# Kernel optimization log

Hardware: AMD Instinct MI355X
Metric: run time of the kernel (lower is better)

The kernel has to match this reference:

```python
import jax, jax.numpy as jnp
import numpy as np

N, E = 50000, 800000
H, C_IN, C_HID, C_OUT = 4, 256, 64, 64
NEG_SLOPE = 0.2


def leaky_relu(x, s=NEG_SLOPE):
    return jnp.where(x >= 0, x, s * x)


def gat_conv(x, src, dst, W, att_src, att_dst, bias, n_nodes):
    # x: [N, F_in], W: [F_in, H*C], att_*: [1, H, C], bias: [H*C]
    Hh, Cc = att_src.shape[1], att_src.shape[2]
    h = (x @ W).reshape(n_nodes, Hh, Cc)            # [N, H, C]
    a_src = (h * att_src).sum(-1)                   # [N, H]
    a_dst = (h * att_dst).sum(-1)                   # [N, H]
    alpha = leaky_relu(a_src[src] + a_dst[dst])     # [E, H]
    # segment softmax over incoming edges of each destination node
    m = jax.ops.segment_max(alpha, dst, num_segments=n_nodes)   # [N, H]
    e = jnp.exp(alpha - m[dst])                     # [E, H]
    denom = jax.ops.segment_sum(e, dst, num_segments=n_nodes)   # [N, H]
    w = e / jnp.clip(denom, 1e-16)[dst]             # [E, H]
    out = jax.ops.segment_sum(w[:, :, None] * h[src], dst, num_segments=n_nodes)
    return out.reshape(n_nodes, Hh * Cc) + bias


def setup_inputs() -> dict:
    key = jax.random.key(0)
    ks = jax.random.split(key, 10)
    glorot = lambda k, shp: jax.random.normal(k, shp, jnp.float32) * np.sqrt(2.0 / (shp[0] + shp[-1]))
    return {
        "x": jax.random.normal(ks[0], (N, C_IN), jnp.float32),
        "edge_index": jax.random.randint(ks[1], (2, E), 0, N, jnp.int32),
        "W1": glorot(ks[2], (C_IN, H * C_HID)),
        "att_src1": glorot(ks[3], (1, H, C_HID)),
        "att_dst1": glorot(ks[4], (1, H, C_HID)),
        "b1": jnp.zeros((H * C_HID,), jnp.float32),
        "W2": glorot(ks[5], (H * C_HID, H * C_OUT)),
        "att_src2": glorot(ks[6], (1, H, C_OUT)),
        "att_dst2": glorot(ks[7], (1, H, C_OUT)),
        "b2": jnp.zeros((H * C_OUT,), jnp.float32),
    }


def reference(x, edge_index, W1, att_src1, att_dst1, b1, W2, att_src2, att_dst2, b2):
    n = x.shape[0]
    loops = jnp.arange(n, dtype=edge_index.dtype)
    src = jnp.concatenate([edge_index[0], loops])
    dst = jnp.concatenate([edge_index[1], loops])
    h1 = gat_conv(x, src, dst, W1, att_src1, att_dst1, b1, n)
    h1 = jax.nn.relu(h1)
    out = gat_conv(h1, src, dst, W2, att_src2, att_dst2, b2, n)
    return out
```

## Files before the change

### kernel.cpp

```cpp
#include <hip/hip_runtime.h>
#include <math.h>

#define NEG_SLOPE 0.2f

typedef __attribute__((ext_vector_type(8))) short bf16x8;
typedef __attribute__((ext_vector_type(4))) float f32x4;
typedef __attribute__((ext_vector_type(4))) unsigned short u16x4;
typedef __attribute__((ext_vector_type(8))) unsigned short u16x8;

static __device__ __forceinline__ f32x4 lky4(f32x4 v) {
    f32x4 r;
    r.x = v.x >= 0.f ? v.x : NEG_SLOPE * v.x;
    r.y = v.y >= 0.f ? v.y : NEG_SLOPE * v.y;
    r.z = v.z >= 0.f ? v.z : NEG_SLOPE * v.z;
    r.w = v.w >= 0.f ? v.w : NEG_SLOPE * v.w;
    return r;
}
static __device__ __forceinline__ f32x4 exp4(f32x4 v) {
    f32x4 r;
    r.x = __expf(v.x); r.y = __expf(v.y); r.z = __expf(v.z); r.w = __expf(v.w);
    return r;
}
static __device__ __forceinline__ float bf2f(unsigned short u) {
    return __uint_as_float(((unsigned int)u) << 16);
}
static __device__ __forceinline__ unsigned short f2bf_rne(float f) {
    unsigned int u = __float_as_uint(f);
    u += 0x7fffu + ((u >> 16) & 1u);
    return (unsigned short)(u >> 16);
}


__global__ void hist_kernel(const int* __restrict__ dst, int* __restrict__ counts, int E, int Nn) {
    int i = blockIdx.x * blockDim.x + threadIdx.x;
    int tot = E + Nn;
    if (i < tot) {
        int d = (i < E) ? dst[i] : (i - E);
        atomicAdd(&counts[d], 1);
    }
}

__global__ void scan1_kernel(const int* __restrict__ counts, int* __restrict__ partial,
                             int* __restrict__ blockSums, int Nn) {
    __shared__ int sh[1024];
    int b = blockIdx.x, t = threadIdx.x;
    int base = b * 1024;
    int orig[4];
    for (int r = 0; r < 4; r++) {
        int i = t + r * 256;
        int v = (base + i < Nn) ? counts[base + i] : 0;
        orig[r] = v;
        sh[i] = v;
    }
    __syncthreads();
    for (int off = 1; off < 1024; off <<= 1) {
        int vals[4];
        for (int r = 0; r < 4; r++) { int i = t + r * 256; vals[r] = (i >= off) ? sh[i - off] : 0; }
        __syncthreads();
        for (int r = 0; r < 4; r++) { int i = t + r * 256; sh[i] += vals[r]; }
        __syncthreads();
    }
    for (int r = 0; r < 4; r++) {
        int i = t + r * 256;
        if (base + i < Nn) partial[base + i] = sh[i] - orig[r];
    }
    if (t == 0) blockSums[b] = sh[1023];
}

__global__ void scan2_kernel(int* __restrict__ blockSums, int nb) {
    if (threadIdx.x == 0 && blockIdx.x == 0) {
        int s = 0;
        for (int i = 0; i < nb; i++) { int v = blockSums[i]; blockSums[i] = s; s += v; }
    }
}

__global__ void finalize_kernel(const int* __restrict__ partial, const int* __restrict__ blockOff,
                                int* __restrict__ row_ptr, int Nn, int Etot) {
    int i = blockIdx.x * blockDim.x + threadIdx.x;
    if (i < Nn) row_ptr[i] = partial[i] + blockOff[i >> 10];
    if (i == 0) row_ptr[Nn] = Etot;
}

__global__ void scatter_kernel(const int* __restrict__ srcE, const int* __restrict__ dstE,
                               const int* __restrict__ row_ptr, int* __restrict__ fill,
                               int* __restrict__ srcs, int E, int Nn) {
    int i = blockIdx.x * blockDim.x + threadIdx.x;
    int tot = E + Nn;
    if (i < tot) {
        int s, d;
        if (i < E) { s = srcE[i]; d = dstE[i]; }
        else       { s = d = i - E; }
        int pos = row_ptr[d] + atomicAdd(&fill[d], 1);
        srcs[pos] = s;
    }
}

__global__ void convertA_kernel(const float* __restrict__ X, unsigned short* __restrict__ Ab,
                                int rows) {
    int t = blockIdx.x * 256 + threadIdx.x;
    if (t >= rows * 64) return;
    int r = t >> 6, c4 = t & 63;
    f32x4 v = *((const f32x4*)(X + ((size_t)r << 8)) + c4);
    u16x4 o;
    o.x = f2bf_rne(v.x); o.y = f2bf_rne(v.y);
    o.z = f2bf_rne(v.z); o.w = f2bf_rne(v.w);
    *(u16x4*)(Ab + (size_t)r * 256 + c4 * 4) = o;
}

__global__ void transposeW_kernel(const float* __restrict__ W, unsigned short* __restrict__ Bt) {
    int t = blockIdx.x * 256 + threadIdx.x;
    int n = t >> 8, k = t & 255;
    Bt[(size_t)n * 256 + k] = f2bf_rne(W[k * 256 + n]);
}

__global__ __launch_bounds__(256) void gemm_kernel(const unsigned short* __restrict__ Ab,
                                                   const unsigned short* __restrict__ Bt,
                                                   unsigned short* __restrict__ Gb,
                                                   int rows) {
    __shared__ __align__(128) unsigned char smem[65536];

    int tid = threadIdx.x;
    int lane = tid & 63, wid = tid >> 6;
    int wr = wid >> 1, wc = wid & 1;
    int bm = blockIdx.x * 128;
    int bn = blockIdx.y * 128;

    f32x4 zero4 = {0.f, 0.f, 0.f, 0.f};
    f32x4 acc[4][4];
#pragma unroll
    for (int i = 0; i < 4; i++)
#pragma unroll
        for (int j = 0; j < 4; j++) acc[i][j] = zero4;

    int sr = tid >> 3;
    int sc = tid & 7;

    auto stage = [&](int kt, int buf) {
        unsigned short* As = (unsigned short*)(smem + buf * 32768);
        unsigned short* Bs = As + 8192;
#pragma unroll
        for (int q = 0; q < 4; q++) {
            int rt = q * 32 + sr;
            int gr = bm + rt; if (gr >= rows) gr = rows - 1;
            int cg = sc ^ (rt & 7);
            const unsigned short* gp = Ab + (size_t)gr * 256 + kt + cg * 8;
            unsigned short* lp = As + rt * 64 + sc * 8;
            __builtin_amdgcn_global_load_lds(
                (__attribute__((address_space(1))) void*)(uintptr_t)gp,
                (__attribute__((address_space(3))) void*)lp, 16, 0, 0);
        }
#pragma unroll
        for (int q = 0; q < 4; q++) {
            int rt = q * 32 + sr;
            int gn = bn + rt;
            int cg = sc ^ (rt & 7);
            const unsigned short* gp = Bt + (size_t)gn * 256 + kt + cg * 8;
            unsigned short* lp = Bs + rt * 64 + sc * 8;
            __builtin_amdgcn_global_load_lds(
                (__attribute__((address_space(1))) void*)(uintptr_t)gp,
                (__attribute__((address_space(3))) void*)lp, 16, 0, 0);
        }
    };

    stage(0, 0);
    __syncthreads();

    for (int kt = 0; kt < 4; kt++) {
        if (kt < 3) stage((kt + 1) * 64, (kt + 1) & 1);
        unsigned short* As = (unsigned short*)(smem + (kt & 1) * 32768);
        unsigned short* Bs = As + 8192;
#pragma unroll
        for (int ks = 0; ks < 2; ks++) {
            bf16x8 af[4], bfr[4];
#pragma unroll
            for (int f = 0; f < 4; f++) {
                int r = wr * 64 + f * 16 + (lane & 15);
                int c = (ks * 4 + (lane >> 4)) ^ (r & 7);
                af[f] = *(const bf16x8*)(As + r * 64 + c * 8);
                int rb = wc * 64 + f * 16 + (lane & 15);
                int cb = (ks * 4 + (lane >> 4)) ^ (rb & 7);
                bfr[f] = *(const bf16x8*)(Bs + rb * 64 + cb * 8);
            }
#pragma unroll
            for (int i = 0; i < 4; i++)
#pragma unroll
                for (int j = 0; j < 4; j++)
                    acc[i][j] = __builtin_amdgcn_mfma_f32_16x16x32_bf16(af[i], bfr[j], acc[i][j], 0, 0, 0);
        }
        __syncthreads();
    }

    int r0 = wr * 64 + (lane >> 4) * 4;
    int c0 = wc * 64 + (lane & 15);
#pragma unroll
    for (int i = 0; i < 4; i++) {
#pragma unroll
        for (int j = 0; j < 4; j++) {
#pragma unroll
            for (int rg = 0; rg < 4; rg++) {
                int lr = bm + r0 + i * 16 + rg;
                if (lr < rows) {
                    int col = bn + c0 + j * 16;
                    Gb[(size_t)lr * 256 + col] = f2bf_rne(acc[i][j][rg]);
                }
            }
        }
    }
}

__global__ __launch_bounds__(256) void attn_kernel(const unsigned short* __restrict__ Gb,
                                                   const float* __restrict__ att_s,
                                                   const float* __restrict__ att_d,
                                                   float* __restrict__ a_src,
                                                   float* __restrict__ a_dst, int N) {
    int wv = threadIdx.x >> 6, lane = threadIdx.x & 63;
    int n = blockIdx.x * 4 + wv;
    if (n >= N) return;
    u16x4 g4 = *(const u16x4*)(Gb + (size_t)n * 256 + lane * 4);
    f32x4 g;
    g.x = bf2f(g4.x); g.y = bf2f(g4.y); g.z = bf2f(g4.z); g.w = bf2f(g4.w);
    f32x4 s4 = ((const f32x4*)att_s)[lane];
    f32x4 d4 = ((const f32x4*)att_d)[lane];
    f32x4 p = g * s4, q = g * d4;
    float ps = p.x + p.y + p.z + p.w;
    float pd = q.x + q.y + q.z + q.w;
#pragma unroll
    for (int off = 1; off < 16; off <<= 1) {
        ps += __shfl_xor(ps, off);
        pd += __shfl_xor(pd, off);
    }
    if ((lane & 15) == 0) {
        int head = lane >> 4;
        a_src[n * 4 + head] = ps;
        a_dst[n * 4 + head] = pd;
    }
}

__global__ __launch_bounds__(256) void gather_kernel(const unsigned short* __restrict__ Gb,
                                                     const float* __restrict__ a_src,
                                                     const float* __restrict__ a_dst,
                                                     const int* __restrict__ row_ptr,
                                                     const int* __restrict__ srcs,
                                                     const float* __restrict__ bias,
                                                     float* __restrict__ outF,
                                                     unsigned short* __restrict__ outB,
                                                     int N) {
    __shared__ int s_lds[4][64];
    __shared__ f32x4 w_lds[4][64];
    int wv = threadIdx.x >> 6, lane = threadIdx.x & 63;
    int n = blockIdx.x * 4 + wv;
    if (n >= N) return;
    int half = lane >> 5;
    int sl = lane & 31;
    int head = sl >> 3;

    int start = row_ptr[n], end = row_ptr[n + 1];
    const f32x4* as4p = (const f32x4*)a_src;
    f32x4 adn4 = *(const f32x4*)(a_dst + (size_t)n * 4);

    float acc[8] = {0.f, 0.f, 0.f, 0.f, 0.f, 0.f, 0.f, 0.f};
    f32x4 dsum4 = {0.f, 0.f, 0.f, 0.f};

    for (int c0 = start; c0 < end; c0 += 64) {
        int cnt = min(64, end - c0);
        if (lane < cnt) {
            int s = srcs[c0 + lane];
            f32x4 ev = exp4(lky4(as4p[s] + adn4));
            s_lds[wv][lane] = s;
            w_lds[wv][lane] = ev;
            dsum4 += ev;
        }

        int j = 0;
        for (; j + 7 < cnt; j += 8) {
            int e0 = j + half, e1 = j + 2 + half, e2 = j + 4 + half, e3 = j + 6 + half;
            int s0 = s_lds[wv][e0];
            int s1 = s_lds[wv][e1];
            int s2 = s_lds[wv][e2];
            int s3 = s_lds[wv][e3];
            float w0 = ((const float*)&w_lds[wv][e0])[head];
            float w1 = ((const float*)&w_lds[wv][e1])[head];
            float w2 = ((const float*)&w_lds[wv][e2])[head];
            float w3 = ((const float*)&w_lds[wv][e3])[head];
            u16x8 g0 = *(const u16x8*)(Gb + (size_t)s0 * 256 + sl * 8);
            u16x8 g1 = *(const u16x8*)(Gb + (size_t)s1 * 256 + sl * 8);
            u16x8 g2 = *(const u16x8*)(Gb + (size_t)s2 * 256 + sl * 8);
            u16x8 g3 = *(const u16x8*)(Gb + (size_t)s3 * 256 + sl * 8);
#pragma unroll
            for (int k = 0; k < 8; k++) {
                acc[k] = fmaf(bf2f(g0[k]), w0, acc[k]);
                acc[k] = fmaf(bf2f(g1[k]), w1, acc[k]);
                acc[k] = fmaf(bf2f(g2[k]), w2, acc[k]);
                acc[k] = fmaf(bf2f(g3[k]), w3, acc[k]);
            }
        }
        for (; j < cnt; j += 2) {
            int e = j + half;
            if (e < cnt) {
                int s0 = s_lds[wv][e];
                float w0 = ((const float*)&w_lds[wv][e])[head];
                u16x8 g0 = *(const u16x8*)(Gb + (size_t)s0 * 256 + sl * 8);
#pragma unroll
                for (int k = 0; k < 8; k++)
                    acc[k] = fmaf(bf2f(g0[k]), w0, acc[k]);
            }
        }
    }

#pragma unroll
    for (int k = 0; k < 8; k++) acc[k] += __shfl_xor(acc[k], 32);
#pragma unroll
    for (int off = 32; off; off >>= 1) {
        dsum4.x += __shfl_xor(dsum4.x, off);
        dsum4.y += __shfl_xor(dsum4.y, off);
        dsum4.z += __shfl_xor(dsum4.z, off);
        dsum4.w += __shfl_xor(dsum4.w, off);
    }
    float den = head == 0 ? dsum4.x : head == 1 ? dsum4.y : head == 2 ? dsum4.z : dsum4.w;
    float rden = 1.0f / den;

    float r[8];
    const float* bp = bias + sl * 8;
#pragma unroll
    for (int k = 0; k < 8; k++) r[k] = acc[k] * rden + bp[k];

    if (outF) {
        if (half == 0) {
            f32x4 v0 = {r[0], r[1], r[2], r[3]};
            f32x4 v1 = {r[4], r[5], r[6], r[7]};
            f32x4* op = (f32x4*)(outF + (size_t)n * 256 + sl * 8);
            op[0] = v0; op[1] = v1;
        }
    } else {
        if (half == 0) {
            u16x8 v;
#pragma unroll
            for (int k = 0; k < 8; k++) v[k] = f2bf_rne(fmaxf(r[k], 0.f));
            *(u16x8*)(outB + (size_t)n * 256 + sl * 8) = v;
        }
    }
}


extern "C" void kernel_launch(void* const* d_in, const int* in_sizes, int n_in,
                              void* d_out, int out_size, void* d_ws, size_t ws_size,
                              hipStream_t stream) {
    const float* x   = (const float*)d_in[0];
    const int*   ei  = (const int*)d_in[1];
    const float* W1  = (const float*)d_in[2];
    const float* as1 = (const float*)d_in[3];
    const float* ad1 = (const float*)d_in[4];
    const float* b1  = (const float*)d_in[5];
    const float* W2  = (const float*)d_in[6];
    const float* as2 = (const float*)d_in[7];
    const float* ad2 = (const float*)d_in[8];
    const float* b2  = (const float*)d_in[9];

    int N = in_sizes[0] / 256;
    int E = in_sizes[1] / 2;
    int Etot = E + N;
    const int* srcE = ei;
    const int* dstE = ei + E;
    float* out = (float*)d_out;

    char* w = (char*)d_ws;
    size_t used = 0;
    auto alloc = [&](size_t bytes) -> char* {
        char* p = w + used;
        used += (bytes + 255) & ~(size_t)255;
        return p;
    };
    unsigned short* Gb = (unsigned short*)alloc((size_t)N * 256 * 2);
    unsigned short* Ab = (unsigned short*)alloc((size_t)N * 256 * 2);
    float* a_src   = (float*)alloc((size_t)N * 4 * 4);
    float* a_dst   = (float*)alloc((size_t)N * 4 * 4);
    int* counts    = (int*)alloc((size_t)N * 4);
    int* partial   = (int*)alloc((size_t)N * 4);
    int* row_ptr   = (int*)alloc(((size_t)N + 1) * 4);
    int* srcs      = (int*)alloc((size_t)Etot * 4);
    int* blockSums = (int*)alloc(256 * 4);
    unsigned short* Bt = (unsigned short*)alloc((size_t)256 * 256 * 2);

    hipMemsetAsync(counts, 0, (size_t)N * 4, stream);

    hist_kernel<<<(Etot + 255) / 256, 256, 0, stream>>>(dstE, counts, E, N);
    int nScanBlocks = (N + 1023) / 1024;
    scan1_kernel<<<nScanBlocks, 256, 0, stream>>>(counts, partial, blockSums, N);
    scan2_kernel<<<1, 64, 0, stream>>>(blockSums, nScanBlocks);
    finalize_kernel<<<(N + 255) / 256, 256, 0, stream>>>(partial, blockSums, row_ptr, N, Etot);
    hipMemsetAsync(counts, 0, (size_t)N * 4, stream);
    scatter_kernel<<<(Etot + 255) / 256, 256, 0, stream>>>(srcE, dstE, row_ptr, counts, srcs, E, N);

    int nodeBlocks = (N + 3) / 4;
    dim3 gg((N + 127) / 128, 2);

    convertA_kernel<<<(N * 64 + 255) / 256, 256, 0, stream>>>(x, Ab, N);
    transposeW_kernel<<<256, 256, 0, stream>>>(W1, Bt);
    gemm_kernel<<<gg, 256, 0, stream>>>(Ab, Bt, Gb, N);
    attn_kernel<<<nodeBlocks, 256, 0, stream>>>(Gb, as1, ad1, a_src, a_dst, N);
    gather_kernel<<<nodeBlocks, 256, 0, stream>>>(Gb, a_src, a_dst, row_ptr, srcs, b1,
                                                  nullptr, Ab, N);

    transposeW_kernel<<<256, 256, 0, stream>>>(W2, Bt);
    gemm_kernel<<<gg, 256, 0, stream>>>(Ab, Bt, Gb, N);
    attn_kernel<<<nodeBlocks, 256, 0, stream>>>(Gb, as2, ad2, a_src, a_dst, N);
    gather_kernel<<<nodeBlocks, 256, 0, stream>>>(Gb, a_src, a_dst, row_ptr, srcs, b2,
                                                  out, nullptr, N);
}
```

Measured before the change: 301.0 us.

## Fuse fp32-to-bf16 conversion into GEMM, degree-sort gather nodes, deepen gather unroll

Removes the separate convertA pass by having the first GEMM load fp32 x and convert to bf16 in registers before writing LDS. Adds a degree-bucket counting sort (hist, scan, scatter kernels) so the gather kernel processes nodes in descending degree order, which balances work across waves. The gather inner loop is also unrolled to 16 edges per iteration to keep more independent loads in flight. The costs are three extra small kernels, a synchronous register path in place of the async global_load_lds for layer 1, and higher register pressure in the gather.

```diff
diff --git a/kernel.cpp b/kernel.cpp
--- a/kernel.cpp
+++ b/kernel.cpp
@@ -95,16 +95,42 @@
     }
 }
 
-__global__ void convertA_kernel(const float* __restrict__ X, unsigned short* __restrict__ Ab,
-                                int rows) {
-    int t = blockIdx.x * 256 + threadIdx.x;
-    if (t >= rows * 64) return;
-    int r = t >> 6, c4 = t & 63;
-    f32x4 v = *((const f32x4*)(X + ((size_t)r << 8)) + c4);
-    u16x4 o;
-    o.x = f2bf_rne(v.x); o.y = f2bf_rne(v.y);
-    o.z = f2bf_rne(v.z); o.w = f2bf_rne(v.w);
-    *(u16x4*)(Ab + (size_t)r * 256 + c4 * 4) = o;
+
+__global__ void deg_hist_kernel(const int* __restrict__ row_ptr, int* __restrict__ bcnt, int Nn) {
+    int i = blockIdx.x * blockDim.x + threadIdx.x;
+    if (i < Nn) {
+        int d = row_ptr[i + 1] - row_ptr[i];
+        int b = 255 - min(d, 255);
+        atomicAdd(&bcnt[b], 1);
+    }
+}
+
+__global__ void deg_scan_kernel(const int* __restrict__ bcnt, int* __restrict__ boff,
+                                int* __restrict__ bfill) {
+    __shared__ int sh[256];
+    int t = threadIdx.x;
+    int orig = bcnt[t];
+    sh[t] = orig;
+    __syncthreads();
+    for (int off = 1; off < 256; off <<= 1) {
+        int v = (t >= off) ? sh[t - off] : 0;
+        __syncthreads();
+        sh[t] += v;
+        __syncthreads();
+    }
+    boff[t] = sh[t] - orig;
+    bfill[t] = 0;
+}
+
+__global__ void deg_scatter_kernel(const int* __restrict__ row_ptr, const int* __restrict__ boff,
+                                   int* __restrict__ bfill, int* __restrict__ node_order, int Nn) {
+    int i = blockIdx.x * blockDim.x + threadIdx.x;
+    if (i < Nn) {
+        int d = row_ptr[i + 1] - row_ptr[i];
+        int b = 255 - min(d, 255);
+        int pos = boff[b] + atomicAdd(&bfill[b], 1);
+        node_order[pos] = i;
+    }
 }
 
 __global__ void transposeW_kernel(const float* __restrict__ W, unsigned short* __restrict__ Bt) {
@@ -113,7 +139,9 @@
     Bt[(size_t)n * 256 + k] = f2bf_rne(W[k * 256 + n]);
 }
 
+template<int F32A>
 __global__ __launch_bounds__(256) void gemm_kernel(const unsigned short* __restrict__ Ab,
+                                                   const float* __restrict__ Xf,
                                                    const unsigned short* __restrict__ Bt,
                                                    unsigned short* __restrict__ Gb,
                                                    int rows) {
@@ -143,11 +171,23 @@
             int rt = q * 32 + sr;
             int gr = bm + rt; if (gr >= rows) gr = rows - 1;
             int cg = sc ^ (rt & 7);
-            const unsigned short* gp = Ab + (size_t)gr * 256 + kt + cg * 8;
-            unsigned short* lp = As + rt * 64 + sc * 8;
-            __builtin_amdgcn_global_load_lds(
-                (__attribute__((address_space(1))) void*)(uintptr_t)gp,
-                (__attribute__((address_space(3))) void*)lp, 16, 0, 0);
+            if (F32A) {
+                const float* xp = Xf + (size_t)gr * 256 + kt + cg * 8;
+                f32x4 a0 = *(const f32x4*)xp;
+                f32x4 a1 = *(const f32x4*)(xp + 4);
+                u16x8 v;
+                v[0] = f2bf_rne(a0.x); v[1] = f2bf_rne(a0.y);
+                v[2] = f2bf_rne(a0.z); v[3] = f2bf_rne(a0.w);
+                v[4] = f2bf_rne(a1.x); v[5] = f2bf_rne(a1.y);
+                v[6] = f2bf_rne(a1.z); v[7] = f2bf_rne(a1.w);
+                *(u16x8*)(As + rt * 64 + sc * 8) = v;
+            } else {
+                const unsigned short* gp = Ab + (size_t)gr * 256 + kt + cg * 8;
+                unsigned short* lp = As + rt * 64 + sc * 8;
+                __builtin_amdgcn_global_load_lds(
+                    (__attribute__((address_space(1))) void*)(uintptr_t)gp,
+                    (__attribute__((address_space(3))) void*)lp, 16, 0, 0);
+            }
         }
 #pragma unroll
         for (int q = 0; q < 4; q++) {
@@ -241,6 +281,7 @@
                                                      const float* __restrict__ a_dst,
                                                      const int* __restrict__ row_ptr,
                                                      const int* __restrict__ srcs,
+                                                     const int* __restrict__ node_order,
                                                      const float* __restrict__ bias,
                                                      float* __restrict__ outF,
                                                      unsigned short* __restrict__ outB,
@@ -248,8 +289,9 @@
     __shared__ int s_lds[4][64];
     __shared__ f32x4 w_lds[4][64];
     int wv = threadIdx.x >> 6, lane = threadIdx.x & 63;
-    int n = blockIdx.x * 4 + wv;
-    if (n >= N) return;
+    int idx = blockIdx.x * 4 + wv;
+    if (idx >= N) return;
+    int n = node_order[idx];
     int half = lane >> 5;
     int sl = lane & 31;
     int head = sl >> 3;
@@ -272,27 +314,41 @@
         }
 
         int j = 0;
+        for (; j + 15 < cnt; j += 16) {
+            int sv_[8]; float wv_[8];
+#pragma unroll
+            for (int t = 0; t < 8; t++) {
+                int e = j + 2 * t + half;
+                sv_[t] = s_lds[wv][e];
+                wv_[t] = ((const float*)&w_lds[wv][e])[head];
+            }
+            u16x8 gv_[8];
+#pragma unroll
+            for (int t = 0; t < 8; t++)
+                gv_[t] = *(const u16x8*)(Gb + (size_t)sv_[t] * 256 + sl * 8);
+#pragma unroll
+            for (int t = 0; t < 8; t++)
+#pragma unroll
+                for (int k = 0; k < 8; k++)
+                    acc[k] = fmaf(bf2f(gv_[t][k]), wv_[t], acc[k]);
+        }
         for (; j + 7 < cnt; j += 8) {
-            int e0 = j + half, e1 = j + 2 + half, e2 = j + 4 + half, e3 = j + 6 + half;
-            int s0 = s_lds[wv][e0];
-            int s1 = s_lds[wv][e1];
-            int s2 = s_lds[wv][e2];
-            int s3 = s_lds[wv][e3];
-            float w0 = ((const float*)&w_lds[wv][e0])[head];
-            float w1 = ((const float*)&w_lds[wv][e1])[head];
-            float w2 = ((const float*)&w_lds[wv][e2])[head];
-            float w3 = ((const float*)&w_lds[wv][e3])[head];
-            u16x8 g0 = *(const u16x8*)(Gb + (size_t)s0 * 256 + sl * 8);
-            u16x8 g1 = *(const u16x8*)(Gb + (size_t)s1 * 256 + sl * 8);
-            u16x8 g2 = *(const u16x8*)(Gb + (size_t)s2 * 256 + sl * 8);
-            u16x8 g3 = *(const u16x8*)(Gb + (size_t)s3 * 256 + sl * 8);
-#pragma unroll
-            for (int k = 0; k < 8; k++) {
-                acc[k] = fmaf(bf2f(g0[k]), w0, acc[k]);
-                acc[k] = fmaf(bf2f(g1[k]), w1, acc[k]);
-                acc[k] = fmaf(bf2f(g2[k]), w2, acc[k]);
-                acc[k] = fmaf(bf2f(g3[k]), w3, acc[k]);
-            }
+            int sv_[4]; float wv_[4];
+#pragma unroll
+            for (int t = 0; t < 4; t++) {
+                int e = j + 2 * t + half;
+                sv_[t] = s_lds[wv][e];
+                wv_[t] = ((const float*)&w_lds[wv][e])[head];
+            }
+            u16x8 gv_[4];
+#pragma unroll
+            for (int t = 0; t < 4; t++)
+                gv_[t] = *(const u16x8*)(Gb + (size_t)sv_[t] * 256 + sl * 8);
+#pragma unroll
+            for (int t = 0; t < 4; t++)
+#pragma unroll
+                for (int k = 0; k < 8; k++)
+                    acc[k] = fmaf(bf2f(gv_[t][k]), wv_[t], acc[k]);
         }
         for (; j < cnt; j += 2) {
             int e = j + half;
@@ -378,10 +434,15 @@
     int* partial   = (int*)alloc((size_t)N * 4);
     int* row_ptr   = (int*)alloc(((size_t)N + 1) * 4);
     int* srcs      = (int*)alloc((size_t)Etot * 4);
+    int* node_order= (int*)alloc((size_t)N * 4);
     int* blockSums = (int*)alloc(256 * 4);
+    int* bcnt      = (int*)alloc(256 * 4);
+    int* boff      = (int*)alloc(256 * 4);
+    int* bfill     = (int*)alloc(256 * 4);
     unsigned short* Bt = (unsigned short*)alloc((size_t)256 * 256 * 2);
 
     hipMemsetAsync(counts, 0, (size_t)N * 4, stream);
+    hipMemsetAsync(bcnt, 0, 256 * 4, stream);
 
     hist_kernel<<<(Etot + 255) / 256, 256, 0, stream>>>(dstE, counts, E, N);
     int nScanBlocks = (N + 1023) / 1024;
@@ -391,19 +452,22 @@
     hipMemsetAsync(counts, 0, (size_t)N * 4, stream);
     scatter_kernel<<<(Etot + 255) / 256, 256, 0, stream>>>(srcE, dstE, row_ptr, counts, srcs, E, N);
 
+    deg_hist_kernel<<<(N + 255) / 256, 256, 0, stream>>>(row_ptr, bcnt, N);
+    deg_scan_kernel<<<1, 256, 0, stream>>>(bcnt, boff, bfill);
+    deg_scatter_kernel<<<(N + 255) / 256, 256, 0, stream>>>(row_ptr, boff, bfill, node_order, N);
+
     int nodeBlocks = (N + 3) / 4;
     dim3 gg((N + 127) / 128, 2);
 
-    convertA_kernel<<<(N * 64 + 255) / 256, 256, 0, stream>>>(x, Ab, N);
     transposeW_kernel<<<256, 256, 0, stream>>>(W1, Bt);
-    gemm_kernel<<<gg, 256, 0, stream>>>(Ab, Bt, Gb, N);
+    gemm_kernel<1><<<gg, 256, 0, stream>>>(nullptr, x, Bt, Gb, N);
     attn_kernel<<<nodeBlocks, 256, 0, stream>>>(Gb, as1, ad1, a_src, a_dst, N);
-    gather_kernel<<<nodeBlocks, 256, 0, stream>>>(Gb, a_src, a_dst, row_ptr, srcs, b1,
-                                                  nullptr, Ab, N);
+    gather_kernel<<<nodeBlocks, 256, 0, stream>>>(Gb, a_src, a_dst, row_ptr, srcs, node_order,
+                                                  b1, nullptr, Ab, N);
 
     transposeW_kernel<<<256, 256, 0, stream>>>(W2, Bt);
-    gemm_kernel<<<gg, 256, 0, stream>>>(Ab, Bt, Gb, N);
+    gemm_kernel<0><<<gg, 256, 0, stream>>>(Ab, nullptr, Bt, Gb, N);
     attn_kernel<<<nodeBlocks, 256, 0, stream>>>(Gb, as2, ad2, a_src, a_dst, N);
-    gather_kernel<<<nodeBlocks, 256, 0, stream>>>(Gb, a_src, a_dst, row_ptr, srcs, b2,
-                                                  out, nullptr, N);
-}
+    gather_kernel<<<nodeBlocks, 256, 0, stream>>>(Gb, a_src, a_dst, row_ptr, srcs, node_order,
+                                                  b2, out, nullptr, N);
+}
```

Result: slower. 596.4 us (+98.2%).
